# Kernel tuning notes

Hardware: AMD Instinct MI355X
Metric: run time of the kernel (lower is better)

The kernel has to match this reference:

```python
import jax, jax.numpy as jnp
import numpy as np

IN_F = 4096
OUT_F = 4096
RANK = 16
NUM_SLOTS = 32
ALPHA = 1.0


def setup_inputs() -> dict:
    key = jax.random.key(0)
    k_x, k_w, k_b, k_a, k_bm, k_idx = jax.random.split(key, 6)
    x = jax.random.normal(k_x, (8, 2048, IN_F), dtype=jnp.float32)
    weight = jax.random.normal(k_w, (OUT_F, IN_F), dtype=jnp.float32) * (1.0 / np.sqrt(IN_F))
    bias = jax.random.normal(k_b, (OUT_F,), dtype=jnp.float32) * 0.01
    lora_A = jax.random.normal(k_a, (NUM_SLOTS, IN_F, RANK), dtype=jnp.float32) * 1e-4
    lora_B = jax.random.normal(k_bm, (NUM_SLOTS, RANK, OUT_F), dtype=jnp.float32) * 1e-4
    lora_indices = jax.random.randint(k_idx, (8,), 0, NUM_SLOTS)
    return {"x": x, "weight": weight, "bias": bias, "lora_A": lora_A,
            "lora_B": lora_B, "lora_indices": lora_indices}


def reference(x, weight, bias, lora_A, lora_B, lora_indices):
    # base linear: x @ W.T + b
    out = jnp.einsum('bsd,od->bso', x, weight) + bias
    # per-sample LoRA slot gather + low-rank bmm chain
    chosen_A = lora_A[lora_indices]          # [B, in, r]
    chosen_B = lora_B[lora_indices]          # [B, r, out]
    inter = jnp.einsum('bsd,bdr->bsr', x, chosen_A)       # [B, S, r]
    out_lora = jnp.einsum('bsr,bro->bso', inter, chosen_B)  # [B, S, out]
    return out + ALPHA * out_lora
```

## Files before the change

### kernel.cpp

```cpp
#include <hip/hip_runtime.h>
#include <hip/hip_bf16.h>


#define M_TOT 16384
#define K_TOT 4096
#define N_TOT 4096
#define RANK 16
#define NT2 64

typedef __attribute__((ext_vector_type(8))) short bf16x8;
typedef __attribute__((ext_vector_type(4))) float f32x4;

__device__ __forceinline__ unsigned short f2bf(float f) {
  unsigned int u = __builtin_bit_cast(unsigned int, f);
  u += 0x7fffu + ((u >> 16) & 1u);
  return (unsigned short)(u >> 16);
}

__global__ void cvt_bf16_kernel(const float* __restrict__ src,
                                unsigned short* __restrict__ dst, int n4) {
  int i = blockIdx.x * blockDim.x + threadIdx.x;
  const int stride = gridDim.x * blockDim.x;
  for (; i < n4; i += stride) {
    const float4 v = reinterpret_cast<const float4*>(src)[i];
    ushort4 o;
    o.x = f2bf(v.x); o.y = f2bf(v.y); o.z = f2bf(v.z); o.w = f2bf(v.w);
    reinterpret_cast<ushort4*>(dst)[i] = o;
  }
}

__global__ __launch_bounds__(256) void fused_xcvt_inter_kernel(
    const float* __restrict__ x,
    const float* __restrict__ loraA,
    const int* __restrict__ idx,
    unsigned short* __restrict__ xb,
    float* __restrict__ inter) {
  __shared__ float red[4][16][17];
  const int lane = threadIdx.x & 63;
  const int wq = threadIdx.x >> 6;
  const int m0 = blockIdx.x * 16;
  const int slot = idx[m0 >> 11];
  const int q = lane >> 4;
  const int c = lane & 15;
  const int k0 = wq * 1024;
  const float* __restrict__ xrow = x + (size_t)(m0 + c) * K_TOT + k0 + q * 8;
  unsigned short* __restrict__ xbrow = xb + (size_t)(m0 + c) * K_TOT + k0 + q * 8;
  const float* __restrict__ Abase = loraA + (size_t)slot * K_TOT * RANK + c;

  f32x4 acc = (f32x4){0.f, 0.f, 0.f, 0.f};
#pragma unroll 4
  for (int kt = 0; kt < 1024; kt += 32) {
    const float4 xv0 = *reinterpret_cast<const float4*>(xrow + kt);
    const float4 xv1 = *reinterpret_cast<const float4*>(xrow + kt + 4);
    bf16x8 af;
    af[0] = (short)f2bf(xv0.x); af[1] = (short)f2bf(xv0.y);
    af[2] = (short)f2bf(xv0.z); af[3] = (short)f2bf(xv0.w);
    af[4] = (short)f2bf(xv1.x); af[5] = (short)f2bf(xv1.y);
    af[6] = (short)f2bf(xv1.z); af[7] = (short)f2bf(xv1.w);
    *reinterpret_cast<bf16x8*>(xbrow + kt) = af;
    const float* __restrict__ Ak = Abase + (size_t)(k0 + kt + q * 8) * RANK;
    bf16x8 bfr;
#pragma unroll
    for (int j = 0; j < 8; ++j) bfr[j] = (short)f2bf(Ak[(size_t)j * RANK]);
    acc = __builtin_amdgcn_mfma_f32_16x16x32_bf16(af, bfr, acc, 0, 0, 0);
  }
#pragma unroll
  for (int i = 0; i < 4; ++i) red[wq][q * 4 + i][c] = acc[i];
  __syncthreads();
  if (wq == 0) {
#pragma unroll
    for (int i = 0; i < 4; ++i) {
      const int row = q * 4 + i;
      inter[(size_t)(m0 + row) * RANK + c] =
          red[0][row][c] + red[1][row][c] + red[2][row][c] + red[3][row][c];
    }
  }
}

__device__ __forceinline__ void gload16(const void* g, void* l) {
  __builtin_amdgcn_global_load_lds(
      (const __attribute__((address_space(1))) unsigned int*)g,
      (__attribute__((address_space(3))) unsigned int*)l, 16, 0, 0);
}

#define GBARRIER() asm volatile("s_barrier" ::: "memory")
#define RD(p) (*reinterpret_cast<const bf16x8*>(p))

__global__ __launch_bounds__(512, 2) void gemm_fused_kernel(
    const unsigned short* __restrict__ xb,
    const unsigned short* __restrict__ wb,
    const float* __restrict__ bias,
    const float* __restrict__ inter,
    const float* __restrict__ loraB,
    const int* __restrict__ idx,
    float* __restrict__ out) {
  __shared__ unsigned short lds[2][32768];
  char* ldsB = (char*)&lds[0][0];

  const int tid = threadIdx.x;
  const int lane = tid & 63;
  const int wv = tid >> 6;
  const int wr = wv >> 2;
  const int wc = wv & 3;

  const int bid = ((blockIdx.x & 7) << 7) | (blockIdx.x >> 3);
  const int m0 = (bid >> 4) << 8;
  const int n0 = (bid & 15) << 8;

  const int r0 = tid >> 3;
  const int scol = ((tid & 7) ^ (r0 & 7)) << 3;
  const unsigned short* xsrc = xb + (size_t)(m0 + r0) * K_TOT + scol;
  const unsigned short* wsrc = wb + (size_t)(n0 + r0) * K_TOT + scol;
  const int stg = tid << 4;

#define STAGE64(t)                                                       \
  do {                                                                   \
    const int _bo = (((t) & 1) << 16);                                   \
    const size_t _ko = (size_t)(t) * 64;                                 \
    gload16(xsrc + _ko,                        ldsB + _bo + stg);        \
    gload16(xsrc + (size_t)64  * K_TOT + _ko,  ldsB + _bo + 8192 + stg); \
    gload16(xsrc + (size_t)128 * K_TOT + _ko,  ldsB + _bo + 16384 + stg);\
    gload16(xsrc + (size_t)192 * K_TOT + _ko,  ldsB + _bo + 24576 + stg);\
    gload16(wsrc + _ko,                        ldsB + _bo + 32768 + stg);\
    gload16(wsrc + (size_t)64  * K_TOT + _ko,  ldsB + _bo + 40960 + stg);\
    gload16(wsrc + (size_t)128 * K_TOT + _ko,  ldsB + _bo + 49152 + stg);\
    gload16(wsrc + (size_t)192 * K_TOT + _ko,  ldsB + _bo + 57344 + stg);\
  } while (0)

  const int rl = lane & 15;
  const int q = lane >> 4;
  const int swz = rl & 7;
  const int aoff0 = (wr * 128 + rl) * 128 + ((q ^ swz) << 4);
  const int aoff1 = (wr * 128 + rl) * 128 + (((4 + q) ^ swz) << 4);
  const int boff0 = 32768 + (wc * 64 + rl) * 128 + ((q ^ swz) << 4);
  const int boff1 = 32768 + (wc * 64 + rl) * 128 + (((4 + q) ^ swz) << 4);

  f32x4 acc[8][4];
#pragma unroll
  for (int i = 0; i < 8; ++i)
#pragma unroll
    for (int j = 0; j < 4; ++j) acc[i][j] = (f32x4){0.f, 0.f, 0.f, 0.f};

  STAGE64(0);
  asm volatile("s_waitcnt vmcnt(0)" ::: "memory");
  GBARRIER();

#pragma unroll 1
  for (int t = 0; t < NT2; ++t) {
    const char* base = ldsB + ((t & 1) << 16);
    bf16x8 af[8], bfr0[4], bfr1[4];

#pragma unroll
    for (int nf = 0; nf < 4; ++nf) bfr0[nf] = RD(base + boff0 + nf * 2048);
#pragma unroll
    for (int mf = 0; mf < 8; ++mf) af[mf] = RD(base + aoff0 + mf * 2048);
#pragma unroll
    for (int nf = 0; nf < 4; ++nf) bfr1[nf] = RD(base + boff1 + nf * 2048);
    if (t < NT2 - 1) STAGE64(t + 1);

    asm volatile("s_waitcnt lgkmcnt(4)" ::: "memory");
    __builtin_amdgcn_sched_barrier(0);
    __builtin_amdgcn_s_setprio(1);
#pragma unroll
    for (int mf = 0; mf < 8; ++mf)
#pragma unroll
      for (int nf = 0; nf < 4; ++nf)
        acc[mf][nf] = __builtin_amdgcn_mfma_f32_16x16x32_bf16(
            af[mf], bfr0[nf], acc[mf][nf], 0, 0, 0);
    __builtin_amdgcn_s_setprio(0);
    __builtin_amdgcn_sched_barrier(0);

#pragma unroll
    for (int mf = 0; mf < 8; ++mf) af[mf] = RD(base + aoff1 + mf * 2048);
    asm volatile("s_waitcnt lgkmcnt(0)" ::: "memory");
    __builtin_amdgcn_sched_barrier(0);
    __builtin_amdgcn_s_setprio(1);
#pragma unroll
    for (int mf = 0; mf < 8; ++mf)
#pragma unroll
      for (int nf = 0; nf < 4; ++nf)
        acc[mf][nf] = __builtin_amdgcn_mfma_f32_16x16x32_bf16(
            af[mf], bfr1[nf], acc[mf][nf], 0, 0, 0);
    __builtin_amdgcn_s_setprio(0);
    __builtin_amdgcn_sched_barrier(0);

    asm volatile("s_waitcnt vmcnt(0)" ::: "memory");
    GBARRIER();
  }

  const int slot = idx[m0 >> 11];
  const float* __restrict__ Bmat = loraB + (size_t)slot * RANK * N_TOT;
  const int gn0 = n0 + wc * 64 + rl;

  float bcv[4][RANK];
  float bv[4];
#pragma unroll
  for (int nf = 0; nf < 4; ++nf) {
    const int gn = gn0 + nf * 16;
    bv[nf] = bias[gn];
#pragma unroll
    for (int p = 0; p < RANK; ++p) bcv[nf][p] = Bmat[(size_t)p * N_TOT + gn];
  }
#pragma unroll
  for (int mf = 0; mf < 8; ++mf) {
    const int gmb = m0 + wr * 128 + mf * 16 + (q << 2);
#pragma unroll
    for (int r = 0; r < 4; ++r) {
      const int gm = gmb + r;
      const float4* ivp = reinterpret_cast<const float4*>(inter + (size_t)gm * RANK);
      const float4 iv0 = ivp[0], iv1 = ivp[1], iv2 = ivp[2], iv3 = ivp[3];
      float* orow = out + (size_t)gm * N_TOT;
#pragma unroll
      for (int nf = 0; nf < 4; ++nf) {
        const float lora =
            iv0.x * bcv[nf][0]  + iv0.y * bcv[nf][1]  + iv0.z * bcv[nf][2]  + iv0.w * bcv[nf][3] +
            iv1.x * bcv[nf][4]  + iv1.y * bcv[nf][5]  + iv1.z * bcv[nf][6]  + iv1.w * bcv[nf][7] +
            iv2.x * bcv[nf][8]  + iv2.y * bcv[nf][9]  + iv2.z * bcv[nf][10] + iv2.w * bcv[nf][11] +
            iv3.x * bcv[nf][12] + iv3.y * bcv[nf][13] + iv3.z * bcv[nf][14] + iv3.w * bcv[nf][15];
        orow[gn0 + nf * 16] = acc[mf][nf][r] + bv[nf] + lora;
      }
    }
  }
#undef STAGE64
}

extern "C" void kernel_launch(void* const* d_in, const int* in_sizes, int n_in,
                              void* d_out, int out_size, void* d_ws, size_t ws_size,
                              hipStream_t stream) {
  const float* x     = (const float*)d_in[0];
  const float* w     = (const float*)d_in[1];
  const float* bias  = (const float*)d_in[2];
  const float* loraA = (const float*)d_in[3];
  const float* loraB = (const float*)d_in[4];
  const int*   idx   = (const int*)d_in[5];
  float* out = (float*)d_out;

  char* ws = (char*)d_ws;
  unsigned short* xb   = (unsigned short*)ws;
  unsigned short* wbuf = (unsigned short*)(ws + 134217728);
  float* inter = (float*)(ws + 134217728 + 33554432);

  fused_xcvt_inter_kernel<<<M_TOT / 16, 256, 0, stream>>>(x, loraA, idx, xb, inter);
  cvt_bf16_kernel<<<1024, 256, 0, stream>>>(w, wbuf, N_TOT * K_TOT / 4);
  gemm_fused_kernel<<<(M_TOT / 256) * (N_TOT / 256), 512, 0, stream>>>(
      xb, wbuf, bias, inter, loraB, idx, out);
}
```

Before: 643.7 us.

## Split K-tile MFMA loop into four barrier-synchronized phases with smaller A-fragment loads

Restructures the main GEMM loop so each 64-wide K tile is processed in four phases of two M-fragments each, loading only four A fragments per phase instead of eight, with extra workgroup barriers between phases. This cuts register pressure from A fragments and interleaves LDS reads with MFMA bursts across waves, in the style of ping-pong scheduling. The cost is many more barriers per iteration, which can stall waves if the phases are not balanced.

Result: slower. 714.8 us (+11.1%).

```diff
diff --git a/kernel.cpp b/kernel.cpp
--- a/kernel.cpp
+++ b/kernel.cpp
@@ -6,7 +6,6 @@
 #define K_TOT 4096
 #define N_TOT 4096
 #define RANK 16
-#define NT2 64
 
 typedef __attribute__((ext_vector_type(8))) short bf16x8;
 typedef __attribute__((ext_vector_type(4))) float f32x4;
@@ -113,18 +112,16 @@
   const unsigned short* wsrc = wb + (size_t)(n0 + r0) * K_TOT + scol;
   const int stg = tid << 4;
 
-#define STAGE64(t)                                                       \
-  do {                                                                   \
-    const int _bo = (((t) & 1) << 16);                                   \
-    const size_t _ko = (size_t)(t) * 64;                                 \
-    gload16(xsrc + _ko,                        ldsB + _bo + stg);        \
-    gload16(xsrc + (size_t)64  * K_TOT + _ko,  ldsB + _bo + 8192 + stg); \
-    gload16(xsrc + (size_t)128 * K_TOT + _ko,  ldsB + _bo + 16384 + stg);\
-    gload16(xsrc + (size_t)192 * K_TOT + _ko,  ldsB + _bo + 24576 + stg);\
-    gload16(wsrc + _ko,                        ldsB + _bo + 32768 + stg);\
-    gload16(wsrc + (size_t)64  * K_TOT + _ko,  ldsB + _bo + 40960 + stg);\
-    gload16(wsrc + (size_t)128 * K_TOT + _ko,  ldsB + _bo + 49152 + stg);\
-    gload16(wsrc + (size_t)192 * K_TOT + _ko,  ldsB + _bo + 57344 + stg);\
+#define STAGE_T(BOFS, KO)                                                     \
+  do {                                                                        \
+    gload16(xsrc + (KO),                        ldsB + (BOFS) + stg);         \
+    gload16(xsrc + (size_t)64  * K_TOT + (KO),  ldsB + (BOFS) + 8192 + stg);  \
+    gload16(xsrc + (size_t)128 * K_TOT + (KO),  ldsB + (BOFS) + 16384 + stg); \
+    gload16(xsrc + (size_t)192 * K_TOT + (KO),  ldsB + (BOFS) + 24576 + stg); \
+    gload16(wsrc + (KO),                        ldsB + (BOFS) + 32768 + stg); \
+    gload16(wsrc + (size_t)64  * K_TOT + (KO),  ldsB + (BOFS) + 40960 + stg); \
+    gload16(wsrc + (size_t)128 * K_TOT + (KO),  ldsB + (BOFS) + 49152 + stg); \
+    gload16(wsrc + (size_t)192 * K_TOT + (KO),  ldsB + (BOFS) + 57344 + stg); \
   } while (0)
 
   const int rl = lane & 15;
@@ -141,51 +138,72 @@
 #pragma unroll
     for (int j = 0; j < 4; ++j) acc[i][j] = (f32x4){0.f, 0.f, 0.f, 0.f};
 
-  STAGE64(0);
+  bf16x8 bfr0[4], bfr1[4], afr[4];
+
+#define PH_MFMA(MF)                                                        \
+  do {                                                                     \
+    _Pragma("unroll")                                                      \
+    for (int nf = 0; nf < 4; ++nf) {                                       \
+      acc[(MF)][nf] = __builtin_amdgcn_mfma_f32_16x16x32_bf16(             \
+          afr[0], bfr0[nf], acc[(MF)][nf], 0, 0, 0);                       \
+      acc[(MF)][nf] = __builtin_amdgcn_mfma_f32_16x16x32_bf16(             \
+          afr[1], bfr1[nf], acc[(MF)][nf], 0, 0, 0);                       \
+      acc[(MF) + 1][nf] = __builtin_amdgcn_mfma_f32_16x16x32_bf16(         \
+          afr[2], bfr0[nf], acc[(MF) + 1][nf], 0, 0, 0);                   \
+      acc[(MF) + 1][nf] = __builtin_amdgcn_mfma_f32_16x16x32_bf16(         \
+          afr[3], bfr1[nf], acc[(MF) + 1][nf], 0, 0, 0);                   \
+    }                                                                      \
+  } while (0)
+
+  STAGE_T(0, 0);
   asm volatile("s_waitcnt vmcnt(0)" ::: "memory");
   GBARRIER();
 
 #pragma unroll 1
-  for (int t = 0; t < NT2; ++t) {
-    const char* base = ldsB + ((t & 1) << 16);
-    bf16x8 af[8], bfr0[4], bfr1[4];
-
-#pragma unroll
-    for (int nf = 0; nf < 4; ++nf) bfr0[nf] = RD(base + boff0 + nf * 2048);
-#pragma unroll
-    for (int mf = 0; mf < 8; ++mf) af[mf] = RD(base + aoff0 + mf * 2048);
-#pragma unroll
-    for (int nf = 0; nf < 4; ++nf) bfr1[nf] = RD(base + boff1 + nf * 2048);
-    if (t < NT2 - 1) STAGE64(t + 1);
-
-    asm volatile("s_waitcnt lgkmcnt(4)" ::: "memory");
-    __builtin_amdgcn_sched_barrier(0);
-    __builtin_amdgcn_s_setprio(1);
-#pragma unroll
-    for (int mf = 0; mf < 8; ++mf)
-#pragma unroll
-      for (int nf = 0; nf < 4; ++nf)
-        acc[mf][nf] = __builtin_amdgcn_mfma_f32_16x16x32_bf16(
-            af[mf], bfr0[nf], acc[mf][nf], 0, 0, 0);
-    __builtin_amdgcn_s_setprio(0);
-    __builtin_amdgcn_sched_barrier(0);
-
-#pragma unroll
-    for (int mf = 0; mf < 8; ++mf) af[mf] = RD(base + aoff1 + mf * 2048);
+  for (int t = 0; t < 64; ++t) {
+    const int bofs = (t & 1) << 16;
+    const int nbofs = ((t + 1) & 1) << 16;
+    const size_t ko = (size_t)(t + 1) * 64;
+    const bool st = t < 63;
+
+#pragma unroll
+    for (int nf = 0; nf < 4; ++nf) bfr0[nf] = RD(ldsB + bofs + boff0 + nf * 2048);
+#pragma unroll
+    for (int nf = 0; nf < 4; ++nf) bfr1[nf] = RD(ldsB + bofs + boff1 + nf * 2048);
+    afr[0] = RD(ldsB + bofs + aoff0);
+    afr[1] = RD(ldsB + bofs + aoff1);
+    afr[2] = RD(ldsB + bofs + aoff0 + 2048);
+    afr[3] = RD(ldsB + bofs + aoff1 + 2048);
+    if (st) STAGE_T(nbofs, ko);
+    asm volatile("s_waitcnt lgkmcnt(8)" ::: "memory");
+    GBARRIER();
     asm volatile("s_waitcnt lgkmcnt(0)" ::: "memory");
     __builtin_amdgcn_sched_barrier(0);
     __builtin_amdgcn_s_setprio(1);
-#pragma unroll
-    for (int mf = 0; mf < 8; ++mf)
-#pragma unroll
-      for (int nf = 0; nf < 4; ++nf)
-        acc[mf][nf] = __builtin_amdgcn_mfma_f32_16x16x32_bf16(
-            af[mf], bfr1[nf], acc[mf][nf], 0, 0, 0);
+    PH_MFMA(0);
     __builtin_amdgcn_s_setprio(0);
     __builtin_amdgcn_sched_barrier(0);
-
-    asm volatile("s_waitcnt vmcnt(0)" ::: "memory");
     GBARRIER();
+
+#pragma unroll
+    for (int ph = 1; ph < 4; ++ph) {
+      const int mf = 2 * ph;
+      afr[0] = RD(ldsB + bofs + aoff0 + mf * 2048);
+      afr[1] = RD(ldsB + bofs + aoff1 + mf * 2048);
+      afr[2] = RD(ldsB + bofs + aoff0 + (mf + 1) * 2048);
+      afr[3] = RD(ldsB + bofs + aoff1 + (mf + 1) * 2048);
+      GBARRIER();
+      asm volatile("s_waitcnt lgkmcnt(0)" ::: "memory");
+      __builtin_amdgcn_sched_barrier(0);
+      __builtin_amdgcn_s_setprio(1);
+      PH_MFMA(mf);
+      __builtin_amdgcn_s_setprio(0);
+      __builtin_amdgcn_sched_barrier(0);
+      if (ph == 3) {
+        asm volatile("s_waitcnt vmcnt(0)" ::: "memory");
+      }
+      GBARRIER();
+    }
   }
 
   const int slot = idx[m0 >> 11];
@@ -221,7 +239,8 @@
       }
     }
   }
-#undef STAGE64
+#undef STAGE_T
+#undef PH_MFMA
 }
 
 extern "C" void kernel_launch(void* const* d_in, const int* in_sizes, int n_in,
```
